# Kernel optimization log

Hardware: AMD Instinct MI355X
Metric: run time of the kernel (lower is better)

The kernel has to match this reference:

```python
import jax, jax.numpy as jnp
import numpy as np

B, TXT, IMG, D, H = 1, 512, 2048, 1024, 16
HD = D // H
MLP = 4 * D
L = TXT + IMG

def _ln(x, s, b, eps=1e-6):
    mu = jnp.mean(x, -1, keepdims=True)
    var = jnp.var(x, -1, keepdims=True)
    return (x - mu) * jax.lax.rsqrt(var + eps) * s + b

def _rms(x, scale, eps=1e-6):
    return x * jax.lax.rsqrt(jnp.mean(x * x, -1, keepdims=True) + eps) * scale

def _rope(x, pe):
    # x: [B,H,L,HD] -> pairs [B,H,L,HD/2,1,2]; pe: [1,1,L,HD/2,2,2]
    xr = x.reshape(x.shape[0], x.shape[1], x.shape[2], -1, 1, 2)
    out = pe[..., 0] * xr[..., 0] + pe[..., 1] * xr[..., 1]
    return out.reshape(x.shape)

def _mod(vec, w, b):
    m = jax.nn.silu(vec) @ w + b  # [B, 6D]
    return jnp.split(m[:, None, :], 6, axis=-1)

def _stream_qkv(x, shift, scale, n1s, n1b, qkv_w, qkv_b, qs, ks):
    xm = (1 + scale) * _ln(x, n1s, n1b) + shift
    qkv = xm @ qkv_w + qkv_b  # [B,L,3D]
    b_, l_ = qkv.shape[0], qkv.shape[1]
    qkv = qkv.reshape(b_, l_, 3, H, HD).transpose(2, 0, 3, 1, 4)  # 'B L (K H D) -> K B H L D'
    q, k, v = qkv[0], qkv[1], qkv[2]
    return _rms(q, qs), _rms(k, ks), v

def _fwd(img, txt, vec, pe,
         img_mod_w, img_mod_b, img_norm1_s, img_norm1_b, img_qkv_w, img_qkv_b,
         img_qscale, img_kscale, img_proj_w, img_proj_b, img_norm2_s, img_norm2_b,
         img_mlp_w1, img_mlp_b1, img_mlp_w2, img_mlp_b2,
         txt_mod_w, txt_mod_b, txt_norm1_s, txt_norm1_b, txt_qkv_w, txt_qkv_b,
         txt_qscale, txt_kscale, txt_proj_w, txt_proj_b, txt_norm2_s, txt_norm2_b,
         txt_mlp_w1, txt_mlp_b1, txt_mlp_w2, txt_mlp_b2):
    i_sh1, i_sc1, i_g1, i_sh2, i_sc2, i_g2 = _mod(vec, img_mod_w, img_mod_b)
    t_sh1, t_sc1, t_g1, t_sh2, t_sc2, t_g2 = _mod(vec, txt_mod_w, txt_mod_b)
    iq, ik, iv = _stream_qkv(img, i_sh1, i_sc1, img_norm1_s, img_norm1_b, img_qkv_w, img_qkv_b, img_qscale, img_kscale)
    tq, tk, tv = _stream_qkv(txt, t_sh1, t_sc1, txt_norm1_s, txt_norm1_b, txt_qkv_w, txt_qkv_b, txt_qscale, txt_kscale)
    q = jnp.concatenate((tq, iq), axis=2)  # txt tokens first
    k = jnp.concatenate((tk, ik), axis=2)
    v = jnp.concatenate((tv, iv), axis=2)
    q = _rope(q, pe)
    k = _rope(k, pe)
    logits = jnp.einsum('bhqd,bhkd->bhqk', q, k) * (HD ** -0.5)
    attn = jnp.einsum('bhqk,bhkd->bhqd', jax.nn.softmax(logits, axis=-1), v)
    attn = attn.transpose(0, 2, 1, 3).reshape(q.shape[0], L, D)  # 'B H L D -> B L (H D)'
    t_attn, i_attn = attn[:, :TXT], attn[:, TXT:]
    img = img + i_g1 * (i_attn @ img_proj_w + img_proj_b)
    h = (1 + i_sc2) * _ln(img, img_norm2_s, img_norm2_b) + i_sh2
    img = img + i_g2 * (jax.nn.gelu(h @ img_mlp_w1 + img_mlp_b1) @ img_mlp_w2 + img_mlp_b2)
    txt = txt + t_g1 * (t_attn @ txt_proj_w + txt_proj_b)
    h = (1 + t_sc2) * _ln(txt, txt_norm2_s, txt_norm2_b) + t_sh2
    txt = txt + t_g2 * (jax.nn.gelu(h @ txt_mlp_w1 + txt_mlp_b1) @ txt_mlp_w2 + txt_mlp_b2)
    return img, txt

def setup_inputs():
    key = jax.random.key(0)
    keys = iter(jax.random.split(key, 80))
    def rn(shape, s=0.02):
        return jax.random.normal(next(keys), shape, jnp.float32) * s
    inp = {
        'img': jax.random.normal(next(keys), (B, IMG, D), jnp.float32),
        'txt': jax.random.normal(next(keys), (B, TXT, D), jnp.float32),
        'vec': jax.random.normal(next(keys), (B, D), jnp.float32),
        'pe': jax.random.normal(next(keys), (1, 1, L, HD // 2, 2, 2), jnp.float32),
    }
    for p in ('img', 'txt'):
        inp[p + '_mod_w'] = rn((D, 6 * D)); inp[p + '_mod_b'] = jnp.zeros((6 * D,), jnp.float32)
        inp[p + '_norm1_s'] = jnp.ones((D,), jnp.float32); inp[p + '_norm1_b'] = jnp.zeros((D,), jnp.float32)
        inp[p + '_qkv_w'] = rn((D, 3 * D)); inp[p + '_qkv_b'] = jnp.zeros((3 * D,), jnp.float32)
        inp[p + '_qscale'] = jnp.ones((HD,), jnp.float32); inp[p + '_kscale'] = jnp.ones((HD,), jnp.float32)
        inp[p + '_proj_w'] = rn((D, D)); inp[p + '_proj_b'] = jnp.zeros((D,), jnp.float32)
        inp[p + '_norm2_s'] = jnp.ones((D,), jnp.float32); inp[p + '_norm2_b'] = jnp.zeros((D,), jnp.float32)
        inp[p + '_mlp_w1'] = rn((D, MLP)); inp[p + '_mlp_b1'] = jnp.zeros((MLP,), jnp.float32)
        inp[p + '_mlp_w2'] = rn((MLP, D)); inp[p + '_mlp_b2'] = jnp.zeros((D,), jnp.float32)
    return inp

def reference(img, txt, vec, pe,
              img_mod_w, img_mod_b, img_norm1_s, img_norm1_b, img_qkv_w, img_qkv_b,
              img_qscale, img_kscale, img_proj_w, img_proj_b, img_norm2_s, img_norm2_b,
              img_mlp_w1, img_mlp_b1, img_mlp_w2, img_mlp_b2,
              txt_mod_w, txt_mod_b, txt_norm1_s, txt_norm1_b, txt_qkv_w, txt_qkv_b,
              txt_qscale, txt_kscale, txt_proj_w, txt_proj_b, txt_norm2_s, txt_norm2_b,
              txt_mlp_w1, txt_mlp_b1, txt_mlp_w2, txt_mlp_b2):
    return _fwd(img, txt, vec, pe,
                img_mod_w, img_mod_b, img_norm1_s, img_norm1_b, img_qkv_w, img_qkv_b,
                img_qscale, img_kscale, img_proj_w, img_proj_b, img_norm2_s, img_norm2_b,
                img_mlp_w1, img_mlp_b1, img_mlp_w2, img_mlp_b2,
                txt_mod_w, txt_mod_b, txt_norm1_s, txt_norm1_b, txt_qkv_w, txt_qkv_b,
                txt_qscale, txt_kscale, txt_proj_w, txt_proj_b, txt_norm2_s, txt_norm2_b,
                txt_mlp_w1, txt_mlp_b1, txt_mlp_w2, txt_mlp_b2)
```

## Files before the change

kernel.cpp:

```cpp
#include <hip/hip_runtime.h>
#include <cstdint>
#include <cstddef>

#define DD 1024
#define HD 64
#define NH 16
#define LTXT 512
#define LIMG 2048
#define LTOT 2560
#define DMLP 4096

typedef unsigned short u16;
typedef __attribute__((ext_vector_type(8))) __bf16 bf16x8;
typedef __attribute__((ext_vector_type(4))) float f32x4;

__device__ __forceinline__ u16 f2bf(float f) {
  union { float f; uint32_t u; } v; v.f = f;
  uint32_t r = v.u + 0x7FFFu + ((v.u >> 16) & 1u);
  return (u16)(r >> 16);
}
__device__ __forceinline__ float bf2f(u16 u) {
  union { uint32_t u; float f; } v; v.u = ((uint32_t)u) << 16;
  return v.f;
}
__device__ __forceinline__ uint32_t cvtpk(float lo, float hi) {
  uint32_t r;
  asm("v_cvt_pk_bf16_f32 %0, %1, %2" : "=v"(r) : "v"(lo), "v"(hi));
  return r;
}
__device__ __forceinline__ float geluf(float x) {
  const float u = fmaf(x * x, 0.044715f, 1.0f);
  const float e = __expf(x * u * -1.5957691216057308f);
  return x / (1.f + e);
}
__device__ __forceinline__ void gload16(const void* g, void* l) {
  __builtin_amdgcn_global_load_lds(
      (const __attribute__((address_space(1))) void*)g,
      (__attribute__((address_space(3))) void*)l, 16, 0, 0);
}
#define SWZ(row) (((((row) & 3) | ((((row) >> 3) & 1) << 2)) << 4))

__global__ __launch_bounds__(256) void wcast_all(
    const float* __restrict__ s0, const float* __restrict__ s1,
    const float* __restrict__ s2, const float* __restrict__ s3,
    const float* __restrict__ s4, const float* __restrict__ s5,
    const float* __restrict__ s6, const float* __restrict__ s7,
    u16* __restrict__ d0, u16* __restrict__ d1, u16* __restrict__ d2,
    u16* __restrict__ d3, u16* __restrict__ d4, u16* __restrict__ d5,
    u16* __restrict__ d6, u16* __restrict__ d7) {
  const int b = blockIdx.x;
  const float* W; u16* Wt; int K, N, lb;
  if (b < 768)       { W = s0; Wt = d0; K = 1024; N = 3072; lb = b; }
  else if (b < 1536) { W = s1; Wt = d1; K = 1024; N = 3072; lb = b - 768; }
  else if (b < 1792) { W = s2; Wt = d2; K = 1024; N = 1024; lb = b - 1536; }
  else if (b < 2048) { W = s3; Wt = d3; K = 1024; N = 1024; lb = b - 1792; }
  else if (b < 3072) { W = s4; Wt = d4; K = 1024; N = 4096; lb = b - 2048; }
  else if (b < 4096) { W = s5; Wt = d5; K = 1024; N = 4096; lb = b - 3072; }
  else if (b < 5120) { W = s6; Wt = d6; K = 4096; N = 1024; lb = b - 4096; }
  else               { W = s7; Wt = d7; K = 4096; N = 1024; lb = b - 5120; }
  const int ntn = N >> 6;
  const int n0 = (lb % ntn) * 64, k0 = (lb / ntn) * 64;
  __shared__ float T[64][65];
  const int tx = threadIdx.x & 15, ty = threadIdx.x >> 4;
#pragma unroll
  for (int i = 0; i < 4; ++i) {
    const int r = ty + i * 16;
    const float4 v = *(const float4*)&W[(size_t)(k0 + r) * N + n0 + tx * 4];
    T[r][tx * 4 + 0] = v.x;
    T[r][tx * 4 + 1] = v.y;
    T[r][tx * 4 + 2] = v.z;
    T[r][tx * 4 + 3] = v.w;
  }
  __syncthreads();
  const int rn = threadIdx.x >> 2;
  const int cs = (threadIdx.x & 3) * 16;
  u16 buf[16];
#pragma unroll
  for (int j = 0; j < 16; ++j) buf[j] = f2bf(T[cs + j][rn]);
  u16* dst = &Wt[(size_t)(n0 + rn) * K + k0 + cs];
  *(uint4*)dst = *(uint4*)&buf[0];
  *(uint4*)(dst + 8) = *(uint4*)&buf[8];
}

__global__ __launch_bounds__(256) void mod_gemv_part(
    const float* __restrict__ vec, const float* __restrict__ wi,
    const float* __restrict__ wt, float* __restrict__ part) {
  __shared__ float sv[128];
  const int s = blockIdx.y, kc = blockIdx.z;
  const float* W = s ? wt : wi;
  if (threadIdx.x < 128) {
    float x = vec[kc * 128 + threadIdx.x];
    sv[threadIdx.x] = x / (1.f + __expf(-x));
  }
  __syncthreads();
  const int j = blockIdx.x * 256 + threadIdx.x;
  float acc = 0.f;
#pragma unroll 4
  for (int i = 0; i < 128; ++i)
    acc += sv[i] * W[(size_t)(kc * 128 + i) * 6144 + j];
  part[((size_t)(kc * 2 + s)) * 6144 + j] = acc;
}
__global__ __launch_bounds__(256) void mod_reduce(
    const float* __restrict__ part, const float* __restrict__ bi,
    const float* __restrict__ bt, float* __restrict__ modout) {
  const int idx = blockIdx.x * 256 + threadIdx.x;
  const int s = idx / 6144, j = idx % 6144;
  float a = s ? bt[j] : bi[j];
#pragma unroll
  for (int kc = 0; kc < 8; ++kc) a += part[((size_t)(kc * 2 + s)) * 6144 + j];
  modout[(size_t)s * 6144 + j] = a;
}

__global__ __launch_bounds__(256) void ln_mod2(
    const float* __restrict__ Xtxt, const float* __restrict__ Ximg,
    u16* __restrict__ out, const float* __restrict__ tns,
    const float* __restrict__ tnb, const float* __restrict__ ins,
    const float* __restrict__ inb, const float* __restrict__ modv) {
  __shared__ float red[8];
  const int r = blockIdx.x, tid = threadIdx.x;
  const float* x; const float* ns; const float* nb; const float* mv;
  if (r < LTXT) { x = Xtxt + (size_t)r * DD; ns = tns; nb = tnb; mv = modv + 6144; }
  else { x = Ximg + (size_t)(r - LTXT) * DD; ns = ins; nb = inb; mv = modv; }
  float v[4];
  float s = 0.f, sq = 0.f;
#pragma unroll
  for (int i = 0; i < 4; ++i) {
    v[i] = x[tid + i * 256];
    s += v[i];
    sq += v[i] * v[i];
  }
#pragma unroll
  for (int o = 32; o; o >>= 1) {
    s += __shfl_xor(s, o);
    sq += __shfl_xor(sq, o);
  }
  if ((tid & 63) == 0) {
    red[tid >> 6] = s;
    red[4 + (tid >> 6)] = sq;
  }
  __syncthreads();
  s = red[0] + red[1] + red[2] + red[3];
  sq = red[4] + red[5] + red[6] + red[7];
  const float mu = s * (1.f / DD);
  const float var = sq * (1.f / DD) - mu * mu;
  const float rstd = rsqrtf(var + 1e-6f);
  u16* o = out + (size_t)r * DD;
#pragma unroll
  for (int i = 0; i < 4; ++i) {
    const int c = tid + i * 256;
    const float ln = (v[i] - mu) * rstd * ns[c] + nb[c];
    o[c] = f2bf((1.f + mv[1024 + c]) * ln + mv[c]);
  }
}

__global__ __launch_bounds__(256) void resid_ln2(
    const float* __restrict__ Xtxt, const float* __restrict__ Ximg,
    const u16* __restrict__ t, const float* __restrict__ modv,
    const float* __restrict__ tns, const float* __restrict__ tnb,
    const float* __restrict__ ins, const float* __restrict__ inb,
    float* __restrict__ otxt, float* __restrict__ oimg,
    u16* __restrict__ hout) {
  __shared__ float red[8];
  const int r = blockIdx.x, tid = threadIdx.x;
  const float* x; const float* ns; const float* nb; const float* mv; float* y;
  if (r < LTXT) {
    x = Xtxt + (size_t)r * DD; ns = tns; nb = tnb; mv = modv + 6144;
    y = otxt + (size_t)r * DD;
  } else {
    x = Ximg + (size_t)(r - LTXT) * DD; ns = ins; nb = inb; mv = modv;
    y = oimg + (size_t)(r - LTXT) * DD;
  }
  const u16* tt = t + (size_t)r * DD;
  float v[4];
  float s = 0.f, sq = 0.f;
#pragma unroll
  for (int i = 0; i < 4; ++i) {
    const int c = tid + i * 256;
    v[i] = x[c] + mv[2048 + c] * bf2f(tt[c]);
    y[c] = v[i];
    s += v[i];
    sq += v[i] * v[i];
  }
#pragma unroll
  for (int o = 32; o; o >>= 1) {
    s += __shfl_xor(s, o);
    sq += __shfl_xor(sq, o);
  }
  if ((tid & 63) == 0) {
    red[tid >> 6] = s;
    red[4 + (tid >> 6)] = sq;
  }
  __syncthreads();
  s = red[0] + red[1] + red[2] + red[3];
  sq = red[4] + red[5] + red[6] + red[7];
  const float mu = s * (1.f / DD);
  const float var = sq * (1.f / DD) - mu * mu;
  const float rstd = rsqrtf(var + 1e-6f);
  u16* o = hout + (size_t)r * DD;
#pragma unroll
  for (int i = 0; i < 4; ++i) {
    const int c = tid + i * 256;
    const float ln = (v[i] - mu) * rstd * ns[c] + nb[c];
    o[c] = f2bf((1.f + mv[4096 + c]) * ln + mv[3072 + c]);
  }
}

__global__ __launch_bounds__(256) void gemm_pipe(
    const u16* __restrict__ A, const u16* __restrict__ BtT,
    const u16* __restrict__ BtI, const float* __restrict__ biasT,
    const float* __restrict__ biasI, u16* __restrict__ C,
    float* __restrict__ Cpart, int K, int Kblk, int N, int gelu) {
  __shared__ __align__(16) u16 As[2][128 * 32];
  __shared__ __align__(16) u16 Bs[2][128 * 32];
  const int tid = threadIdx.x, lane = tid & 63, wave = tid >> 6;
  const int nwg = gridDim.x * gridDim.y;
  const int orig = blockIdx.x + blockIdx.y * gridDim.x;
  const int lb = (orig & 7) * (nwg >> 3) + (orig >> 3);
  const int bn = lb / 20, bm = lb % 20;
  const int kc = blockIdx.z;
  const u16* Bt = (bm < (LTXT / 128)) ? BtT : BtI;
  const int wm = wave >> 1, wn = wave & 1;
  const int lr = lane & 15, lk = lane >> 4;
  f32x4 acc[4][4] = {};
  const size_t a0 = (size_t)bm * 128;
  const size_t b0 = (size_t)bn * 128;
  const int kbase = kc * Kblk;
  const int NT = Kblk >> 5;
  const int srow = lane >> 2, soff = (lane & 3) * 8;

#define STAGE(t, buf)                                                         \
  {                                                                           \
    const int k0_ = kbase + (t) * 32;                                         \
    _Pragma("unroll") for (int j = 0; j < 2; ++j) {                           \
      const int chunk = wave * 2 + j;                                         \
      gload16(&A[(a0 + chunk * 16 + srow) * K + k0_ + soff],                  \
              &As[buf][chunk * 512]);                                         \
      gload16(&Bt[(b0 + chunk * 16 + srow) * K + k0_ + soff],                 \
              &Bs[buf][chunk * 512]);                                         \
    }                                                                         \
  }

  STAGE(0, 0);
  STAGE(1, 1);
  for (int t = 0; t < NT; ++t) {
    if (t + 1 < NT) {
      asm volatile("s_waitcnt vmcnt(4)" ::: "memory");
    } else {
      asm volatile("s_waitcnt vmcnt(0)" ::: "memory");
    }
    __builtin_amdgcn_s_barrier();
    const int b = t & 1;
    bf16x8 af[4], bfv[4];
#pragma unroll
    for (int m = 0; m < 4; ++m)
      af[m] = *(const bf16x8*)&As[b][(wm * 64 + m * 16 + lr) * 32 + lk * 8];
#pragma unroll
    for (int n = 0; n < 4; ++n)
      bfv[n] = *(const bf16x8*)&Bs[b][(wn * 64 + n * 16 + lr) * 32 + lk * 8];
    asm volatile("s_waitcnt lgkmcnt(0)" ::: "memory");
    __builtin_amdgcn_sched_barrier(0);
    __builtin_amdgcn_s_barrier();
    if (t + 2 < NT) STAGE(t + 2, b);
    __builtin_amdgcn_sched_barrier(0);
    __builtin_amdgcn_s_setprio(1);
#pragma unroll
    for (int m = 0; m < 4; ++m)
#pragma unroll
      for (int n = 0; n < 4; ++n)
        acc[m][n] = __builtin_amdgcn_mfma_f32_16x16x32_bf16(af[m], bfv[n],
                                                            acc[m][n], 0, 0, 0);
    __builtin_amdgcn_s_setprio(0);
  }
#undef STAGE

  if (Cpart) {
    float* dst = Cpart + (size_t)kc * ((size_t)LTOT * N);
#pragma unroll
    for (int n = 0; n < 4; ++n) {
      const int col = bn * 128 + wn * 64 + n * 16 + lr;
#pragma unroll
      for (int m = 0; m < 4; ++m)
#pragma unroll
        for (int r = 0; r < 4; ++r) {
          const size_t row = a0 + wm * 64 + m * 16 + lk * 4 + r;
          dst[row * (size_t)N + col] = acc[m][n][r];
        }
    }
  } else {
    const float* bias = (bm < (LTXT / 128)) ? biasT : biasI;
#pragma unroll
    for (int n = 0; n < 4; ++n) {
      const int col = bn * 128 + wn * 64 + n * 16 + lr;
      const float bv = bias[col];
#pragma unroll
      for (int m = 0; m < 4; ++m)
#pragma unroll
        for (int r = 0; r < 4; ++r) {
          const size_t row = a0 + wm * 64 + m * 16 + lk * 4 + r;
          float v = acc[m][n][r] + bv;
          if (gelu) v = geluf(v);
          C[row * (size_t)N + col] = f2bf(v);
        }
    }
  }
}

__global__ __launch_bounds__(256) void gemm_reduce(
    const float* __restrict__ part, const float* __restrict__ bT,
    const float* __restrict__ bI, u16* __restrict__ C, int N, int kcnt) {
  const size_t idx = (size_t)(blockIdx.x * 256 + threadIdx.x) * 4;
  const int row = (int)(idx / N), col = (int)(idx % N);
  float4 a = *(const float4*)&part[idx];
  for (int kc = 1; kc < kcnt; ++kc) {
    const float4 b = *(const float4*)&part[(size_t)kc * LTOT * N + idx];
    a.x += b.x; a.y += b.y; a.z += b.z; a.w += b.w;
  }
  const float* bias = (row < LTXT) ? bT : bI;
  ushort4 o;
  o.x = f2bf(a.x + bias[col]);
  o.y = f2bf(a.y + bias[col + 1]);
  o.z = f2bf(a.z + bias[col + 2]);
  o.w = f2bf(a.w + bias[col + 3]);
  *(ushort4*)&C[idx] = o;
}

__global__ __launch_bounds__(256) void gemm_reduce_gate(
    const float* __restrict__ part, const float* __restrict__ bT,
    const float* __restrict__ bI, const float* __restrict__ modv,
    float* __restrict__ otxt, float* __restrict__ oimg, int kcnt) {
  const size_t idx = (size_t)(blockIdx.x * 256 + threadIdx.x) * 4;
  const int row = (int)(idx >> 10), col = (int)(idx & 1023);
  float4 a = *(const float4*)&part[idx];
  for (int kc = 1; kc < kcnt; ++kc) {
    const float4 b = *(const float4*)&part[(size_t)kc * LTOT * DD + idx];
    a.x += b.x; a.y += b.y; a.z += b.z; a.w += b.w;
  }
  const float* bias; const float* mv; float* o;
  if (row < LTXT) {
    bias = bT; mv = modv + 6144; o = otxt + (size_t)row * DD + col;
  } else {
    bias = bI; mv = modv; o = oimg + (size_t)(row - LTXT) * DD + col;
  }
  const float4 g = *(const float4*)&mv[5120 + col];
  const float4 cur = *(const float4*)o;
  float4 r;
  r.x = cur.x + g.x * (a.x + bias[col]);
  r.y = cur.y + g.y * (a.y + bias[col + 1]);
  r.z = cur.z + g.z * (a.z + bias[col + 2]);
  r.w = cur.w + g.w * (a.w + bias[col + 3]);
  *(float4*)o = r;
}

__global__ __launch_bounds__(256) void scat_rope(
    const u16* __restrict__ qkv, u16* __restrict__ q, u16* __restrict__ k,
    const float* __restrict__ pe, const float* __restrict__ iqs,
    const float* __restrict__ iks, const float* __restrict__ tqs,
    const float* __restrict__ tks) {
  const int gw = (blockIdx.x * 256 + threadIdx.x) >> 6;
  const int lane = threadIdx.x & 63;
  const int l = gw % LTOT, h = gw / LTOT;
  const size_t rb = (size_t)l * 3072 + h * 64 + lane;
  const float qv = bf2f(qkv[rb]);
  const float kv = bf2f(qkv[rb + 1024]);
  const float* qs = (l < LTXT) ? tqs : iqs;
  const float* ks = (l < LTXT) ? tks : iks;
  const float* peb = pe + (size_t)l * 128 + (lane >> 1) * 4 + (lane & 1) * 2;
  const size_t base = ((size_t)h * LTOT + l) * HD + lane;
  {
    float ss = qv * qv;
#pragma unroll
    for (int o = 32; o; o >>= 1) ss += __shfl_xor(ss, o);
    float xn = qv * rsqrtf(ss * (1.f / HD) + 1e-6f) * qs[lane];
    float part = __shfl_xor(xn, 1);
    float x0 = (lane & 1) ? part : xn;
    float x1 = (lane & 1) ? xn : part;
    q[base] = f2bf(peb[0] * x0 + peb[1] * x1);
  }
  {
    float ss = kv * kv;
#pragma unroll
    for (int o = 32; o; o >>= 1) ss += __shfl_xor(ss, o);
    float xn = kv * rsqrtf(ss * (1.f / HD) + 1e-6f) * ks[lane];
    float part = __shfl_xor(xn, 1);
    float x0 = (lane & 1) ? part : xn;
    float x1 = (lane & 1) ? xn : part;
    k[base] = f2bf(peb[0] * x0 + peb[1] * x1);
  }
}

__global__ __launch_bounds__(256) void vt_build(const u16* __restrict__ qkv,
                                                u16* __restrict__ vt) {
  __shared__ u16 T[64][72];
  const int b = blockIdx.x;
  const int h = b & 15, lt = b >> 4;
  const int tid = threadIdx.x;
  const int r = tid >> 3, c8 = (tid & 7) * 8;
  const size_t srcbase = (size_t)(lt * 64) * 3072 + 2048 + h * 64;
  *(uint4*)&T[r][c8] = *(const uint4*)&qkv[srcbase + (size_t)r * 3072 + c8];
  *(uint4*)&T[r + 32][c8] =
      *(const uint4*)&qkv[srcbase + (size_t)(r + 32) * 3072 + c8];
  __syncthreads();
  const int d = tid >> 2, lc = (tid & 3) * 16;
  u16 buf[16];
#pragma unroll
  for (int j = 0; j < 16; ++j) buf[j] = T[lc + j][d];
  u16* dst = &vt[((size_t)h * 64 + d) * LTOT + lt * 64 + lc];
  *(uint4*)dst = *(uint4*)&buf[0];
  *(uint4*)(dst + 8) = *(uint4*)&buf[8];
}

template <int SPLIT>
__global__ __launch_bounds__(256) void attn_mfma(
    const u16* __restrict__ Q, const u16* __restrict__ Kg,
    const u16* __restrict__ VT, u16* __restrict__ out,
    float* __restrict__ part) {
  __shared__ __align__(16) u16 Ks[2][64 * 64];
  __shared__ __align__(16) u16 Vs[2][64 * 64];
  const int tid = threadIdx.x, lane = tid & 63, w = tid >> 6;
  const int lr = lane & 15, lk = lane >> 4;
  const int blk = blockIdx.x;
  const int h = ((blk & 7) << 1) | ((blk >> 3) & 1);
  const int half = (SPLIT == 2) ? ((blk >> 4) & 1) : 0;
  const int q0 = (SPLIT == 2 ? (blk >> 5) : (blk >> 4)) * 64;
  const size_t hb = (size_t)h * LTOT;
  char* KsB0 = (char*)&Ks[0][0];
  char* VsB0 = (char*)&Vs[0][0];

  const int q = q0 + w * 16 + lr;
  const bf16x8 qa0 = *(const bf16x8*)&Q[(hb + q) * HD + lk * 8];
  const bf16x8 qa1 = *(const bf16x8*)&Q[(hb + q) * HD + 32 + lk * 8];

  const int srow = tid >> 3;
  const int soff = tid & 7;
  const int NT = (LTOT / SPLIT) / 64;
  const int kstart = half * (LTOT / 2);

  float m_run = -1e30f, l_run = 0.f;
  f32x4 acc[4] = {};
  uint4 kst[2], vst[2];

#pragma unroll
  for (int i = 0; i < 2; ++i) {
    const int row = srow + i * 32;
    kst[i] = *(const uint4*)&Kg[(hb + kstart + row) * HD + soff * 8];
    vst[i] = *(const uint4*)&VT[((size_t)h * HD + row) * LTOT + kstart + soff * 8];
  }
#pragma unroll
  for (int i = 0; i < 2; ++i) {
    const int row = srow + i * 32;
    *(uint4*)(KsB0 + ((row * 128 + soff * 16) ^ SWZ(row))) = kst[i];
    *(uint4*)(VsB0 + ((row * 128 + soff * 16) ^ SWZ(row))) = vst[i];
  }
  __syncthreads();

  const float scale = 0.125f;
  for (int t = 0; t < NT; ++t) {
    char* KsC = KsB0 + (t & 1) * 8192;
    char* VsC = VsB0 + (t & 1) * 8192;
    if (t + 1 < NT) {
      const int k0n = kstart + (t + 1) * 64;
#pragma unroll
      for (int i = 0; i < 2; ++i) {
        const int row = srow + i * 32;
        kst[i] = *(const uint4*)&Kg[(hb + k0n + row) * HD + soff * 8];
        vst[i] = *(const uint4*)&VT[((size_t)h * HD + row) * LTOT + k0n + soff * 8];
      }
    }
    f32x4 s[4];
    __builtin_amdgcn_s_setprio(1);
#pragma unroll
    for (int g = 0; g < 4; ++g) {
      const int kr = (lr >> 2) * 8 + (g & 1) * 4 + (lr & 3) + (g >> 1) * 32;
      const int sw = SWZ(kr);
      const bf16x8 ka0 = *(const bf16x8*)(KsC + ((kr * 128 + lk * 16) ^ sw));
      const bf16x8 ka1 = *(const bf16x8*)(KsC + ((kr * 128 + 64 + lk * 16) ^ sw));
      f32x4 z = {0.f, 0.f, 0.f, 0.f};
      z = __builtin_amdgcn_mfma_f32_16x16x32_bf16(ka0, qa0, z, 0, 0, 0);
      z = __builtin_amdgcn_mfma_f32_16x16x32_bf16(ka1, qa1, z, 0, 0, 0);
      s[g] = z;
    }
    __builtin_amdgcn_s_setprio(0);
    float tmax = s[0][0];
#pragma unroll
    for (int g = 0; g < 4; ++g)
#pragma unroll
      for (int r = 0; r < 4; ++r) tmax = fmaxf(tmax, s[g][r]);
    tmax = fmaxf(tmax, __shfl_xor(tmax, 16));
    tmax = fmaxf(tmax, __shfl_xor(tmax, 32));
    tmax *= scale;
    if (!__all(tmax <= m_run + 8.f)) {
      const float mnew = fmaxf(m_run, tmax);
      const float alpha = __expf(m_run - mnew);
      l_run *= alpha;
#pragma unroll
      for (int dt = 0; dt < 4; ++dt) {
        acc[dt][0] *= alpha;
        acc[dt][1] *= alpha;
        acc[dt][2] *= alpha;
        acc[dt][3] *= alpha;
      }
      m_run = mnew;
    }
    float p[4][4];
    float psum = 0.f;
#pragma unroll
    for (int g = 0; g < 4; ++g)
#pragma unroll
      for (int r = 0; r < 4; ++r) {
        p[g][r] = __expf(s[g][r] * scale - m_run);
        psum += p[g][r];
      }
    psum += __shfl_xor(psum, 16);
    psum += __shfl_xor(psum, 32);
    l_run += psum;
    union { uint32_t u[4]; bf16x8 v; } pb0, pb1;
    pb0.u[0] = cvtpk(p[0][0], p[0][1]);
    pb0.u[1] = cvtpk(p[0][2], p[0][3]);
    pb0.u[2] = cvtpk(p[1][0], p[1][1]);
    pb0.u[3] = cvtpk(p[1][2], p[1][3]);
    pb1.u[0] = cvtpk(p[2][0], p[2][1]);
    pb1.u[1] = cvtpk(p[2][2], p[2][3]);
    pb1.u[2] = cvtpk(p[3][0], p[3][1]);
    pb1.u[3] = cvtpk(p[3][2], p[3][3]);
    __builtin_amdgcn_s_setprio(1);
#pragma unroll
    for (int dt = 0; dt < 4; ++dt) {
      const int vr = dt * 16 + lr;
      const int sw = SWZ(vr);
      const bf16x8 va0 = *(const bf16x8*)(VsC + ((vr * 128 + lk * 16) ^ sw));
      const bf16x8 va1 = *(const bf16x8*)(VsC + ((vr * 128 + 64 + lk * 16) ^ sw));
      acc[dt] = __builtin_amdgcn_mfma_f32_16x16x32_bf16(va0, pb0.v, acc[dt], 0, 0, 0);
      acc[dt] = __builtin_amdgcn_mfma_f32_16x16x32_bf16(va1, pb1.v, acc[dt], 0, 0, 0);
    }
    __builtin_amdgcn_s_setprio(0);
    if (t + 1 < NT) {
      char* KsN = KsB0 + ((t + 1) & 1) * 8192;
      char* VsN = VsB0 + ((t + 1) & 1) * 8192;
#pragma unroll
      for (int i = 0; i < 2; ++i) {
        const int row = srow + i * 32;
        *(uint4*)(KsN + ((row * 128 + soff * 16) ^ SWZ(row))) = kst[i];
        *(uint4*)(VsN + ((row * 128 + soff * 16) ^ SWZ(row))) = vst[i];
      }
      __syncthreads();
    }
  }
  if (SPLIT == 2) {
    float* pr = part + (((size_t)(half * LTOT) + q) * 16 + h) * 68;
#pragma unroll
    for (int dt = 0; dt < 4; ++dt)
      *(f32x4*)&pr[dt * 16 + lk * 4] = acc[dt];
    if (lk == 0) {
      pr[64] = m_run;
      pr[65] = l_run;
    }
  } else {
    __syncthreads();
    const float inv = 1.f / l_run;
    char* ob = KsB0 + w * 2048;
    const int esw = (lr & 7) << 4;
#pragma unroll
    for (int dt = 0; dt < 4; ++dt) {
      const uint32_t a = cvtpk(acc[dt][0] * inv, acc[dt][1] * inv);
      const uint32_t b2 = cvtpk(acc[dt][2] * inv, acc[dt][3] * inv);
      const int ad = lr * 128 + dt * 32 + lk * 8;
      *(uint32_t*)(ob + (ad ^ esw)) = a;
      *(uint32_t*)(ob + ((ad + 4) ^ esw)) = b2;
    }
    __syncthreads();
    const int row = lane >> 2, ch = lane & 3;
    const int rsw = (row & 7) << 4;
    const uint4 o0 = *(const uint4*)(ob + ((row * 128 + ch * 32) ^ rsw));
    const uint4 o1 = *(const uint4*)(ob + ((row * 128 + ch * 32 + 16) ^ rsw));
    u16* orow = &out[(size_t)(q0 + w * 16 + row) * DD + h * HD + ch * 16];
    *(uint4*)orow = o0;
    *(uint4*)(orow + 8) = o1;
  }
}

__global__ __launch_bounds__(256) void attn_merge(const float* __restrict__ part,
                                                  u16* __restrict__ out) {
  const int idx = blockIdx.x * 256 + threadIdx.x;
  const int d4 = idx & 15, h = (idx >> 4) & 15, q = idx >> 8;
  const size_t base0 = ((size_t)q * 16 + h) * 68;
  const size_t base1 = ((size_t)(LTOT + q) * 16 + h) * 68;
  const float m0 = part[base0 + 64], l0 = part[base0 + 65];
  const float m1 = part[base1 + 64], l1 = part[base1 + 65];
  const float m = fmaxf(m0, m1);
  const float a0 = __expf(m0 - m), a1 = __expf(m1 - m);
  const float inv = 1.f / (l0 * a0 + l1 * a1);
  const float4 x0 = *(const float4*)&part[base0 + d4 * 4];
  const float4 x1 = *(const float4*)&part[base1 + d4 * 4];
  const float s0 = a0 * inv, s1 = a1 * inv;
  uint2 o;
  o.x = cvtpk(x0.x * s0 + x1.x * s1, x0.y * s0 + x1.y * s1);
  o.y = cvtpk(x0.z * s0 + x1.z * s1, x0.w * s0 + x1.w * s1);
  *(uint2*)&out[(size_t)q * DD + h * HD + d4 * 4] = o;
}

__global__ __launch_bounds__(256) void resid_gate(
    const float* __restrict__ xin, const u16* __restrict__ t,
    const float* __restrict__ g, float* __restrict__ out, int n4) {
  const int idx = blockIdx.x * 256 + threadIdx.x;
  if (idx >= n4) return;
  const int col = (idx * 4) & (DD - 1);
  const float4 a = ((const float4*)xin)[idx];
  const ushort4 tb = ((const ushort4*)t)[idx];
  const float4 gg = *(const float4*)&g[col];
  float4 r;
  r.x = a.x + gg.x * bf2f(tb.x);
  r.y = a.y + gg.y * bf2f(tb.y);
  r.z = a.z + gg.z * bf2f(tb.z);
  r.w = a.w + gg.w * bf2f(tb.w);
  ((float4*)out)[idx] = r;
}

extern "C" void kernel_launch(void* const* d_in, const int* in_sizes, int n_in,
                              void* d_out, int out_size, void* d_ws,
                              size_t ws_size, hipStream_t stream) {
  const float* img = (const float*)d_in[0];
  const float* txt = (const float*)d_in[1];
  const float* vec = (const float*)d_in[2];
  const float* pe = (const float*)d_in[3];
  const float* i_mod_w = (const float*)d_in[4];
  const float* i_mod_b = (const float*)d_in[5];
  const float* i_n1s = (const float*)d_in[6];
  const float* i_n1b = (const float*)d_in[7];
  const float* i_qkv_w = (const float*)d_in[8];
  const float* i_qkv_b = (const float*)d_in[9];
  const float* i_qs = (const float*)d_in[10];
  const float* i_ks = (const float*)d_in[11];
  const float* i_proj_w = (const float*)d_in[12];
  const float* i_proj_b = (const float*)d_in[13];
  const float* i_n2s = (const float*)d_in[14];
  const float* i_n2b = (const float*)d_in[15];
  const float* i_w1 = (const float*)d_in[16];
  const float* i_b1 = (const float*)d_in[17];
  const float* i_w2 = (const float*)d_in[18];
  const float* i_b2 = (const float*)d_in[19];
  const float* t_mod_w = (const float*)d_in[20];
  const float* t_mod_b = (const float*)d_in[21];
  const float* t_n1s = (const float*)d_in[22];
  const float* t_n1b = (const float*)d_in[23];
  const float* t_qkv_w = (const float*)d_in[24];
  const float* t_qkv_b = (const float*)d_in[25];
  const float* t_qs = (const float*)d_in[26];
  const float* t_ks = (const float*)d_in[27];
  const float* t_proj_w = (const float*)d_in[28];
  const float* t_proj_b = (const float*)d_in[29];
  const float* t_n2s = (const float*)d_in[30];
  const float* t_n2b = (const float*)d_in[31];
  const float* t_w1 = (const float*)d_in[32];
  const float* t_b1 = (const float*)d_in[33];
  const float* t_w2 = (const float*)d_in[34];
  const float* t_b2 = (const float*)d_in[35];

  const size_t LD = (size_t)LTOT * DD;
  uint8_t* p = (uint8_t*)d_ws;
  float* modb = (float*)p;           p += 64 * 1024;
  float* part = (float*)p;           p += 512 * 1024;
  u16* tqkvT = (u16*)p;              p += (size_t)3072 * 1024 * 2;
  u16* iqkvT = (u16*)p;              p += (size_t)3072 * 1024 * 2;
  u16* tprojT = (u16*)p;             p += (size_t)1024 * 1024 * 2;
  u16* iprojT = (u16*)p;             p += (size_t)1024 * 1024 * 2;
  u16* tw1T = (u16*)p;               p += (size_t)4096 * 1024 * 2;
  u16* iw1T = (u16*)p;               p += (size_t)4096 * 1024 * 2;
  u16* tw2T = (u16*)p;               p += (size_t)1024 * 4096 * 2;
  u16* iw2T = (u16*)p;               p += (size_t)1024 * 4096 * 2;
  u16* actA = (u16*)p;               p += LD * 2;
  u16* actB = (u16*)p;               p += (size_t)LTOT * DMLP * 2;
  u16* actC = (u16*)p;               p += LD * 2 * 3;
  float* gpart = (float*)p;
  const size_t used = (size_t)(p - (uint8_t*)d_ws);
  const size_t avail = ws_size > used ? ws_size - used : 0;
  const size_t attn_part_need = (size_t)2 * LTOT * 16 * 68 * sizeof(float);
  const int attn_split = avail >= attn_part_need ? 2 : 1;
  const int kc_proj = avail >= 2 * LD * sizeof(float) ? 2 : 1;
  const int kc_mlp2 = avail >= 4 * LD * sizeof(float)
                          ? 4
                          : (avail >= 2 * LD * sizeof(float) ? 2 : 1);
  float* out_img = (float*)d_out;
  float* out_txt = out_img + (size_t)LIMG * DD;

  wcast_all<<<6144, 256, 0, stream>>>(t_qkv_w, i_qkv_w, t_proj_w, i_proj_w,
                                      t_w1, i_w1, t_w2, i_w2, tqkvT, iqkvT,
                                      tprojT, iprojT, tw1T, iw1T, tw2T, iw2T);
  mod_gemv_part<<<dim3(24, 2, 8), 256, 0, stream>>>(vec, i_mod_w, t_mod_w, part);
  mod_reduce<<<48, 256, 0, stream>>>(part, i_mod_b, t_mod_b, modb);
  ln_mod2<<<LTOT, 256, 0, stream>>>(txt, img, actA, t_n1s, t_n1b, i_n1s, i_n1b,
                                    modb);
  gemm_pipe<<<dim3(24, 20, 1), 256, 0, stream>>>(actA, tqkvT, iqkvT, t_qkv_b,
                                                 i_qkv_b, actB, nullptr, 1024,
                                                 1024, 3072, 0);
  scat_rope<<<10240, 256, 0, stream>>>(actB, actC, actC + LD, pe, i_qs, i_ks,
                                       t_qs, t_ks);
  vt_build<<<640, 256, 0, stream>>>(actB, actC + 2 * LD);
  if (attn_split == 2) {
    attn_mfma<2><<<1280, 256, 0, stream>>>(actC, actC + LD, actC + 2 * LD,
                                           actA, gpart);
    attn_merge<<<2560, 256, 0, stream>>>(gpart, actA);
  } else {
    attn_mfma<1><<<640, 256, 0, stream>>>(actC, actC + LD, actC + 2 * LD, actA,
                                          nullptr);
  }
  if (kc_proj > 1) {
    gemm_pipe<<<dim3(8, 20, kc_proj), 256, 0, stream>>>(
        actA, tprojT, iprojT, nullptr, nullptr, nullptr, gpart, 1024,
        1024 / kc_proj, 1024, 0);
    gemm_reduce<<<2560, 256, 0, stream>>>(gpart, t_proj_b, i_proj_b, actC,
                                          1024, kc_proj);
  } else {
    gemm_pipe<<<dim3(8, 20, 1), 256, 0, stream>>>(actA, tprojT, iprojT,
                                                  t_proj_b, i_proj_b, actC,
                                                  nullptr, 1024, 1024, 1024, 0);
  }
  resid_ln2<<<LTOT, 256, 0, stream>>>(txt, img, actC, modb, t_n2s, t_n2b,
                                      i_n2s, i_n2b, out_txt, out_img,
                                      actC + LD);
  gemm_pipe<<<dim3(32, 20, 1), 256, 0, stream>>>(actC + LD, tw1T, iw1T, t_b1,
                                                 i_b1, actB, nullptr, 1024,
                                                 1024, 4096, 1);
  if (kc_mlp2 > 1) {
    gemm_pipe<<<dim3(8, 20, kc_mlp2), 256, 0, stream>>>(
        actB, tw2T, iw2T, nullptr, nullptr, nullptr, gpart, 4096,
        4096 / kc_mlp2, 1024, 0);
    gemm_reduce_gate<<<2560, 256, 0, stream>>>(gpart, t_b2, i_b2, modb,
                                               out_txt, out_img, kc_mlp2);
  } else {
    gemm_pipe<<<dim3(8, 20, 1), 256, 0, stream>>>(actB, tw2T, iw2T, t_b2, i_b2,
                                                  actC + 2 * LD, nullptr, 4096,
                                                  4096, 1024, 0);
    resid_gate<<<2048, 256, 0, stream>>>(out_img,
                                         actC + 2 * LD + (size_t)LTXT * DD,
                                         modb + 5120, out_img, LIMG * DD / 4);
    resid_gate<<<512, 256, 0, stream>>>(out_txt, actC + 2 * LD,
                                        modb + 6144 + 5120, out_txt,
                                        LTXT * DD / 4);
  }
}
```

Baseline: 294.2 us.

## Vectorize LN kernels and double attention query tile to 512 threads

The two layernorm/modulation kernels switch from strided scalar accesses to per-thread float4 loads and ushort4 stores over contiguous columns. The attention kernel now runs 8 waves per block covering 128 query rows. Each thread stages one K/V row instead of two, so each K/V tile is shared by twice as many queries and the grid is halved. This cuts global K/V reloads per query but raises registers and work per block, which may reduce occupancy.

```diff
diff --git a/kernel.cpp b/kernel.cpp
--- a/kernel.cpp
+++ b/kernel.cpp
@@ -121,14 +121,12 @@
   const float* x; const float* ns; const float* nb; const float* mv;
   if (r < LTXT) { x = Xtxt + (size_t)r * DD; ns = tns; nb = tnb; mv = modv + 6144; }
   else { x = Ximg + (size_t)(r - LTXT) * DD; ns = ins; nb = inb; mv = modv; }
-  float v[4];
+  const int c0 = tid * 4;
+  const float4 xv = *(const float4*)&x[c0];
+  float v[4] = {xv.x, xv.y, xv.z, xv.w};
   float s = 0.f, sq = 0.f;
 #pragma unroll
-  for (int i = 0; i < 4; ++i) {
-    v[i] = x[tid + i * 256];
-    s += v[i];
-    sq += v[i] * v[i];
-  }
+  for (int i = 0; i < 4; ++i) { s += v[i]; sq += v[i] * v[i]; }
 #pragma unroll
   for (int o = 32; o; o >>= 1) {
     s += __shfl_xor(s, o);
@@ -144,13 +142,23 @@
   const float mu = s * (1.f / DD);
   const float var = sq * (1.f / DD) - mu * mu;
   const float rstd = rsqrtf(var + 1e-6f);
-  u16* o = out + (size_t)r * DD;
+  const float4 nsv = *(const float4*)&ns[c0];
+  const float4 nbv = *(const float4*)&nb[c0];
+  const float4 shv = *(const float4*)&mv[c0];
+  const float4 scv = *(const float4*)&mv[1024 + c0];
+  const float nsa[4] = {nsv.x, nsv.y, nsv.z, nsv.w};
+  const float nba[4] = {nbv.x, nbv.y, nbv.z, nbv.w};
+  const float sha[4] = {shv.x, shv.y, shv.z, shv.w};
+  const float sca[4] = {scv.x, scv.y, scv.z, scv.w};
+  ushort4 o4;
+  u16 ob[4];
 #pragma unroll
   for (int i = 0; i < 4; ++i) {
-    const int c = tid + i * 256;
-    const float ln = (v[i] - mu) * rstd * ns[c] + nb[c];
-    o[c] = f2bf((1.f + mv[1024 + c]) * ln + mv[c]);
-  }
+    const float ln = (v[i] - mu) * rstd * nsa[i] + nba[i];
+    ob[i] = f2bf((1.f + sca[i]) * ln + sha[i]);
+  }
+  o4.x = ob[0]; o4.y = ob[1]; o4.z = ob[2]; o4.w = ob[3];
+  *(ushort4*)&out[(size_t)r * DD + c0] = o4;
 }
 
 __global__ __launch_bounds__(256) void resid_ln2(
@@ -170,17 +178,19 @@
     x = Ximg + (size_t)(r - LTXT) * DD; ns = ins; nb = inb; mv = modv;
     y = oimg + (size_t)(r - LTXT) * DD;
   }
-  const u16* tt = t + (size_t)r * DD;
+  const int c0 = tid * 4;
+  const float4 xv = *(const float4*)&x[c0];
+  const ushort4 tb = *(const ushort4*)&t[(size_t)r * DD + c0];
+  const float4 gv = *(const float4*)&mv[2048 + c0];
   float v[4];
+  v[0] = xv.x + gv.x * bf2f(tb.x);
+  v[1] = xv.y + gv.y * bf2f(tb.y);
+  v[2] = xv.z + gv.z * bf2f(tb.z);
+  v[3] = xv.w + gv.w * bf2f(tb.w);
+  *(float4*)&y[c0] = *(float4*)v;
   float s = 0.f, sq = 0.f;
 #pragma unroll
-  for (int i = 0; i < 4; ++i) {
-    const int c = tid + i * 256;
-    v[i] = x[c] + mv[2048 + c] * bf2f(tt[c]);
-    y[c] = v[i];
-    s += v[i];
-    sq += v[i] * v[i];
-  }
+  for (int i = 0; i < 4; ++i) { s += v[i]; sq += v[i] * v[i]; }
 #pragma unroll
   for (int o = 32; o; o >>= 1) {
     s += __shfl_xor(s, o);
@@ -196,13 +206,23 @@
   const float mu = s * (1.f / DD);
   const float var = sq * (1.f / DD) - mu * mu;
   const float rstd = rsqrtf(var + 1e-6f);
-  u16* o = hout + (size_t)r * DD;
+  const float4 nsv = *(const float4*)&ns[c0];
+  const float4 nbv = *(const float4*)&nb[c0];
+  const float4 shv = *(const float4*)&mv[3072 + c0];
+  const float4 scv = *(const float4*)&mv[4096 + c0];
+  const float nsa[4] = {nsv.x, nsv.y, nsv.z, nsv.w};
+  const float nba[4] = {nbv.x, nbv.y, nbv.z, nbv.w};
+  const float sha[4] = {shv.x, shv.y, shv.z, shv.w};
+  const float sca[4] = {scv.x, scv.y, scv.z, scv.w};
+  ushort4 o4;
+  u16 ob[4];
 #pragma unroll
   for (int i = 0; i < 4; ++i) {
-    const int c = tid + i * 256;
-    const float ln = (v[i] - mu) * rstd * ns[c] + nb[c];
-    o[c] = f2bf((1.f + mv[4096 + c]) * ln + mv[3072 + c]);
-  }
+    const float ln = (v[i] - mu) * rstd * nsa[i] + nba[i];
+    ob[i] = f2bf((1.f + sca[i]) * ln + sha[i]);
+  }
+  o4.x = ob[0]; o4.y = ob[1]; o4.z = ob[2]; o4.w = ob[3];
+  *(ushort4*)&hout[(size_t)r * DD + c0] = o4;
 }
 
 __global__ __launch_bounds__(256) void gemm_pipe(
@@ -410,7 +430,7 @@
 }
 
 template <int SPLIT>
-__global__ __launch_bounds__(256) void attn_mfma(
+__global__ __launch_bounds__(512) void attn_mfma(
     const u16* __restrict__ Q, const u16* __restrict__ Kg,
     const u16* __restrict__ VT, u16* __restrict__ out,
     float* __restrict__ part) {
@@ -421,7 +441,7 @@
   const int blk = blockIdx.x;
   const int h = ((blk & 7) << 1) | ((blk >> 3) & 1);
   const int half = (SPLIT == 2) ? ((blk >> 4) & 1) : 0;
-  const int q0 = (SPLIT == 2 ? (blk >> 5) : (blk >> 4)) * 64;
+  const int q0 = (SPLIT == 2 ? (blk >> 5) : (blk >> 4)) * 128;
   const size_t hb = (size_t)h * LTOT;
   char* KsB0 = (char*)&Ks[0][0];
   char* VsB0 = (char*)&Vs[0][0];
@@ -437,20 +457,12 @@
 
   float m_run = -1e30f, l_run = 0.f;
   f32x4 acc[4] = {};
-  uint4 kst[2], vst[2];
-
-#pragma unroll
-  for (int i = 0; i < 2; ++i) {
-    const int row = srow + i * 32;
-    kst[i] = *(const uint4*)&Kg[(hb + kstart + row) * HD + soff * 8];
-    vst[i] = *(const uint4*)&VT[((size_t)h * HD + row) * LTOT + kstart + soff * 8];
-  }
-#pragma unroll
-  for (int i = 0; i < 2; ++i) {
-    const int row = srow + i * 32;
-    *(uint4*)(KsB0 + ((row * 128 + soff * 16) ^ SWZ(row))) = kst[i];
-    *(uint4*)(VsB0 + ((row * 128 + soff * 16) ^ SWZ(row))) = vst[i];
-  }
+  uint4 kst, vst;
+
+  kst = *(const uint4*)&Kg[(hb + kstart + srow) * HD + soff * 8];
+  vst = *(const uint4*)&VT[((size_t)h * HD + srow) * LTOT + kstart + soff * 8];
+  *(uint4*)(KsB0 + ((srow * 128 + soff * 16) ^ SWZ(srow))) = kst;
+  *(uint4*)(VsB0 + ((srow * 128 + soff * 16) ^ SWZ(srow))) = vst;
   __syncthreads();
 
   const float scale = 0.125f;
@@ -459,12 +471,8 @@
     char* VsC = VsB0 + (t & 1) * 8192;
     if (t + 1 < NT) {
       const int k0n = kstart + (t + 1) * 64;
-#pragma unroll
-      for (int i = 0; i < 2; ++i) {
-        const int row = srow + i * 32;
-        kst[i] = *(const uint4*)&Kg[(hb + k0n + row) * HD + soff * 8];
-        vst[i] = *(const uint4*)&VT[((size_t)h * HD + row) * LTOT + k0n + soff * 8];
-      }
+      kst = *(const uint4*)&Kg[(hb + k0n + srow) * HD + soff * 8];
+      vst = *(const uint4*)&VT[((size_t)h * HD + srow) * LTOT + k0n + soff * 8];
     }
     f32x4 s[4];
     __builtin_amdgcn_s_setprio(1);
@@ -536,12 +544,8 @@
     if (t + 1 < NT) {
       char* KsN = KsB0 + ((t + 1) & 1) * 8192;
       char* VsN = VsB0 + ((t + 1) & 1) * 8192;
-#pragma unroll
-      for (int i = 0; i < 2; ++i) {
-        const int row = srow + i * 32;
-        *(uint4*)(KsN + ((row * 128 + soff * 16) ^ SWZ(row))) = kst[i];
-        *(uint4*)(VsN + ((row * 128 + soff * 16) ^ SWZ(row))) = vst[i];
-      }
+      *(uint4*)(KsN + ((srow * 128 + soff * 16) ^ SWZ(srow))) = kst;
+      *(uint4*)(VsN + ((srow * 128 + soff * 16) ^ SWZ(srow))) = vst;
       __syncthreads();
     }
   }
@@ -696,11 +700,11 @@
                                        t_qs, t_ks);
   vt_build<<<640, 256, 0, stream>>>(actB, actC + 2 * LD);
   if (attn_split == 2) {
-    attn_mfma<2><<<1280, 256, 0, stream>>>(actC, actC + LD, actC + 2 * LD,
-                                           actA, gpart);
+    attn_mfma<2><<<640, 512, 0, stream>>>(actC, actC + LD, actC + 2 * LD,
+                                          actA, gpart);
     attn_merge<<<2560, 256, 0, stream>>>(gpart, actA);
   } else {
-    attn_mfma<1><<<640, 256, 0, stream>>>(actC, actC + LD, actC + 2 * LD, actA,
+    attn_mfma<1><<<320, 512, 0, stream>>>(actC, actC + LD, actC + 2 * LD, actA,
                                           nullptr);
   }
   if (kc_proj > 1) {
```

Measured after the change: 286.9 us. -2.5%, faster.
